# Performance work log

Measured on AMD Instinct MI355X. Metric: run time of the kernel, lower is better.

The kernel has to match this reference:

```python
import jax, jax.numpy as jnp
import numpy as np

B, T, N_EMBD, HEAD = 8, 2048, 1024, 64
NEG_INF = -1e30  # stand-in for float('-inf'), safe under fp16/bf16 after where


def setup_inputs() -> dict:
    key = jax.random.key(0)
    k0, k1, k2, k3 = jax.random.split(key, 4)
    idx = jax.random.normal(k0, (B, T, N_EMBD), dtype=jnp.float32)
    # nn.Linear weights have shape (out_features, in_features)
    Wk = jax.random.normal(k1, (HEAD, N_EMBD), dtype=jnp.float32) * 0.02
    Wq = jax.random.normal(k2, (HEAD, N_EMBD), dtype=jnp.float32) * 0.02
    Wv = jax.random.normal(k3, (HEAD, N_EMBD), dtype=jnp.float32) * 0.02
    return {"idx": idx, "Wk": Wk, "Wq": Wq, "Wv": Wv}


def reference(idx, Wk, Wq, Wv):
    # idx: [B,T,C]; W*: [H,C] (torch Linear layout, y = x @ W.T)
    Tn = idx.shape[1]
    k = jnp.einsum('btc,hc->bth', idx, Wk)
    q = jnp.einsum('btc,hc->bth', idx, Wq)
    v = jnp.einsum('btc,hc->bth', idx, Wv)
    # NOTE: original has NO 1/sqrt(head_size) scaling
    wei = jnp.einsum('bth,bsh->bts', q, k)  # [B,T,T]
    causal = jnp.tril(jnp.ones((Tn, Tn), dtype=bool))  # keep where tril != 0
    wei = jnp.where(causal[None, :, :], wei, NEG_INF)
    # NOTE: original softmaxes over dim=1 (query axis), not the last axis
    wei = jax.nn.softmax(wei, axis=1)
    out = jnp.einsum('bts,bsh->bth', wei, v)  # [B,T,H]
    return out
```

## Files before the change

### kernel.cpp

```cpp
#include <hip/hip_runtime.h>


typedef __attribute__((ext_vector_type(8))) short bf16x8;
typedef __attribute__((ext_vector_type(4))) float f32x4;
typedef unsigned short u16;

#define MFMA(a, b, c) __builtin_amdgcn_mfma_f32_16x16x32_bf16((a), (b), (c), 0, 0, 0)

__device__ __forceinline__ u16 f2bf(float x) {
    unsigned u = __float_as_uint(x);
    u += 0x7fff + ((u >> 16) & 1);
    return (u16)(u >> 16);
}
__device__ __forceinline__ float bf2f(u16 h) {
    return __uint_as_float(((unsigned)h) << 16);
}

#define WH_OFF  0u
#define WL_OFF  (WH_OFF + 192u*1024u*2u)
#define FQH_OFF (WL_OFF + 192u*1024u*2u)
#define FQL_OFF (FQH_OFF + 2u*1024u*1024u)
#define FKH_OFF (FQL_OFF + 2u*1024u*1024u)
#define FKL_OFF (FKH_OFF + 2u*1024u*1024u)
#define VF_OFF  (FKL_OFF + 2u*1024u*1024u)
#define DD_OFF  (VF_OFF + 2u*1024u*1024u)
#define PF_OFF  (DD_OFF + 8u*2048u*4u)

__global__ __launch_bounds__(128) void wsplit_kernel(
    const float* __restrict__ Wk, const float* __restrict__ Wq,
    const float* __restrict__ Wv, u16* __restrict__ FWH, u16* __restrict__ FWL)
{
    const int n = blockIdx.x;
    const int nblk = n >> 4, lr = n & 15;
    const float* src = (n < 64) ? (Wq + (long)n * 1024)
                     : (n < 128) ? (Wk + (long)(n - 64) * 1024)
                                 : (Wv + (long)(n - 128) * 1024);
    const int f = threadIdx.x;
    const int kc = f >> 2, q = f & 3;
    const float4 f0 = *(const float4*)&src[kc * 32 + q * 8];
    const float4 f1 = *(const float4*)&src[kc * 32 + q * 8 + 4];
    const float vs[8] = {f0.x, f0.y, f0.z, f0.w, f1.x, f1.y, f1.z, f1.w};
    bf16x8 hv, lv;
    #pragma unroll
    for (int j = 0; j < 8; ++j) {
        const u16 h = f2bf(vs[j]);
        hv[j] = (short)h;
        lv[j] = (short)f2bf(vs[j] - bf2f(h));
    }
    const long o = ((long)(nblk * 32 + kc) * 64 + q * 16 + lr) * 8;
    *(bf16x8*)&FWH[o] = hv;
    *(bf16x8*)&FWL[o] = lv;
}

__global__ __launch_bounds__(512, 2) void qkv_kernel(
    const float* __restrict__ idx, const u16* __restrict__ FWH, const u16* __restrict__ FWL,
    u16* __restrict__ FQH, u16* __restrict__ FQL,
    u16* __restrict__ FKH, u16* __restrict__ FKL, u16* __restrict__ VF)
{
    __shared__ u16 a_l[2][64 * 136];
    const int tid = threadIdx.x;
    const int w = tid >> 6, lr = tid & 15, quad = (tid >> 4) & 3;
    const int lane = tid & 63;
    const int r0 = blockIdx.x * 64;
    const int b = r0 >> 11, t0 = r0 & 2047;
    const int m0 = (w & 1) * 32;
    const int nbb = (w >> 1) * 3;
    const int sr = tid >> 3, sc = (tid & 7) * 8;
    const float* arow = &idx[(long)(r0 + sr) * 1024 + sc];

    const u16* __restrict__ fwh = &FWH[(long)nbb * 16384 + lane * 8];
    const u16* __restrict__ fwl = &FWL[(long)nbb * 16384 + lane * 8];

    f32x4 acc[2][3] = {};
    float4 pf0, pf1;

    bf16x8 FH0[3][2], FL0[3][2], FH1[3][2], FL1[3][2];
    #pragma unroll
    for (int nf = 0; nf < 3; ++nf) {
        const long nb = (long)nf * 16384;
        FH0[nf][0] = *(const bf16x8*)&fwh[nb];
        FH0[nf][1] = *(const bf16x8*)&fwh[nb + 512];
        FL0[nf][0] = *(const bf16x8*)&fwl[nb];
        FL0[nf][1] = *(const bf16x8*)&fwl[nb + 512];
    }

    pf0 = *(const float4*)(arow);
    pf1 = *(const float4*)(arow + 4);
    {
        const float vs[8] = {pf0.x, pf0.y, pf0.z, pf0.w, pf1.x, pf1.y, pf1.z, pf1.w};
        bf16x8 hv, lv;
        #pragma unroll
        for (int j = 0; j < 8; ++j) {
            const u16 h = f2bf(vs[j]);
            hv[j] = (short)h;
            lv[j] = (short)f2bf(vs[j] - bf2f(h));
        }
        *(bf16x8*)&a_l[0][sr * 136 + sc]      = hv;
        *(bf16x8*)&a_l[0][sr * 136 + 64 + sc] = lv;
    }
    __syncthreads();

    int p = 0;

#define QKV_ITER(IT, FHc, FLc, FHn, FLn)                                      \
    {                                                                         \
        const int it_ = (IT);                                                 \
        if (it_ < 15) {                                                       \
               \
            pf0 = *(const float4*)(arow + it_ * 64 + 64);                     \
            pf1 = *(const float4*)(arow + it_ * 64 + 68);                     \
                                        \
            _Pragma("unroll")                                                 \
            for (int nf = 0; nf < 3; ++nf) {                                  \
                const long nb = (long)nf * 16384 + (long)(it_ + 1) * 1024;    \
                FHn[nf][0] = *(const bf16x8*)&fwh[nb];                        \
                FHn[nf][1] = *(const bf16x8*)&fwh[nb + 512];                  \
                FLn[nf][0] = *(const bf16x8*)&fwl[nb];                        \
                FLn[nf][1] = *(const bf16x8*)&fwl[nb + 512];                  \
            }                                                                 \
        }                                                                     \
        bf16x8 AH[2][2], AL[2][2];                                            \
        _Pragma("unroll")                                                     \
        for (int mi = 0; mi < 2; ++mi) {                                      \
            const int ar = (m0 + mi * 16 + lr) * 136 + quad * 8;              \
            AH[mi][0] = *(const bf16x8*)&a_l[p][ar];                          \
            AH[mi][1] = *(const bf16x8*)&a_l[p][ar + 32];                     \
            AL[mi][0] = *(const bf16x8*)&a_l[p][ar + 64];                     \
            AL[mi][1] = *(const bf16x8*)&a_l[p][ar + 96];                     \
        }                                                                     \
        _Pragma("unroll")                                                     \
        for (int nf = 0; nf < 3; ++nf) {                                      \
            _Pragma("unroll")                                                 \
            for (int mi = 0; mi < 2; ++mi) {                                  \
                f32x4 c = acc[mi][nf];                                        \
                c = MFMA(AH[mi][0], FHc[nf][0], c);                           \
                c = MFMA(AL[mi][0], FHc[nf][0], c);                           \
                c = MFMA(AH[mi][0], FLc[nf][0], c);                           \
                c = MFMA(AH[mi][1], FHc[nf][1], c);                           \
                c = MFMA(AL[mi][1], FHc[nf][1], c);                           \
                c = MFMA(AH[mi][1], FLc[nf][1], c);                           \
                acc[mi][nf] = c;                                              \
            }                                                                 \
        }                                                                     \
        if (it_ < 15) {                                                       \
            const float vs[8] = {pf0.x, pf0.y, pf0.z, pf0.w,                  \
                                 pf1.x, pf1.y, pf1.z, pf1.w};                 \
            bf16x8 hv, lv;                                                    \
            _Pragma("unroll")                                                 \
            for (int j = 0; j < 8; ++j) {                                     \
                const u16 h = f2bf(vs[j]);                                    \
                hv[j] = (short)h;                                             \
                lv[j] = (short)f2bf(vs[j] - bf2f(h));                         \
            }                                                                 \
            *(bf16x8*)&a_l[p ^ 1][sr * 136 + sc]      = hv;                   \
            *(bf16x8*)&a_l[p ^ 1][sr * 136 + 64 + sc] = lv;                   \
            __syncthreads();                                                  \
            p ^= 1;                                                           \
        }                                                                     \
    }

    for (int it2 = 0; it2 < 8; ++it2) {
        QKV_ITER(2 * it2,     FH0, FL0, FH1, FL1);
        QKV_ITER(2 * it2 + 1, FH1, FL1, FH0, FL0);
    }
#undef QKV_ITER

    #pragma unroll
    for (int mi = 0; mi < 2; ++mi) {
        const int tb = t0 + m0 + mi * 16 + quad * 4;
        const int tblk = (t0 + m0 + mi * 16) >> 4;
        #pragma unroll
        for (int nf = 0; nf < 3; ++nf) {
            const int n = (nbb + nf) * 16 + lr;
            const f32x4 a = acc[mi][nf];
            if (n < 128) {
                u16* Hd = (n < 64) ? FQH : FKH;
                u16* Ld = (n < 64) ? FQL : FKL;
                const int h = n & 63;
                const int kc = h >> 5;
                const int lsub = 16 * ((h & 31) >> 3);
                const long base = ((long)(b * 128 + tblk) * 2 + kc) * 512 + (h & 7);
                #pragma unroll
                for (int r = 0; r < 4; ++r) {
                    const float v = a[r];
                    const u16 hi = f2bf(v);
                    const u16 lo = f2bf(v - bf2f(hi));
                    const long o = base + (long)(quad * 4 + r + lsub) * 8;
                    Hd[o] = hi; Ld[o] = lo;
                }
            } else {
                const int h = n - 128;
                const int hblk = h >> 4;
                #pragma unroll
                for (int r = 0; r < 4; ++r) {
                    const int t = tb + r;
                    const long o = ((long)(b * 4 + hblk) * 64 + (t >> 5)) * 512
                                 + (long)(16 * ((t & 31) >> 3) + (h & 15)) * 8 + (t & 7);
                    VF[o] = f2bf(a[r]);
                }
            }
        }
    }
}

__global__ __launch_bounds__(256, 4) void stats_kernel(
    const u16* __restrict__ FQH, const u16* __restrict__ FQL,
    const u16* __restrict__ FKH, const u16* __restrict__ FKL,
    u16* __restrict__ PF, float* __restrict__ D)
{
    __shared__ float red[4][64];
    const int tid = threadIdx.x;
    const int w = tid >> 6, lr = tid & 15, quad = (tid >> 4) & 3;
    const int lane = tid & 63;
    const int b = blockIdx.y;
    int x = blockIdx.x, i = 0;
    for (;;) { const int nc = (35 - i) >> 2; if (x < nc) break; x -= nc; ++i; }
    const int s0 = i * 64;
    const int jt0 = i + 4 * x, jt1 = min(jt0 + 4, 32);

    bf16x8 BH[4][2], BL[4][2];
    #pragma unroll
    for (int nf = 0; nf < 4; ++nf) {
        const long kb = ((long)(b * 128 + i * 4 + nf) * 2) * 512 + lane * 8;
        BH[nf][0] = *(const bf16x8*)&FKH[kb];
        BH[nf][1] = *(const bf16x8*)&FKH[kb + 512];
        BL[nf][0] = *(const bf16x8*)&FKL[kb];
        BL[nf][1] = *(const bf16x8*)&FKL[kb + 512];
    }

    float dsum[4] = {0.f, 0.f, 0.f, 0.f};
    for (int jt = jt0; jt < jt1; ++jt) {
        const long qb = ((long)(b * 128 + jt * 4 + w) * 2) * 512 + lane * 8;
        const bf16x8 ah0 = *(const bf16x8*)&FQH[qb];
        const bf16x8 ah1 = *(const bf16x8*)&FQH[qb + 512];
        const bf16x8 al0 = *(const bf16x8*)&FQL[qb];
        const bf16x8 al1 = *(const bf16x8*)&FQL[qb + 512];
        const bool diag = (jt == i);
        #pragma unroll
        for (int nf = 0; nf < 4; ++nf) {
            f32x4 cc = {};
            cc = MFMA(ah0, BH[nf][0], cc);
            cc = MFMA(al0, BH[nf][0], cc);
            cc = MFMA(ah0, BL[nf][0], cc);
            cc = MFMA(ah1, BH[nf][1], cc);
            cc = MFMA(al1, BH[nf][1], cc);
            cc = MFMA(ah1, BL[nf][1], cc);

            const long pbase = ((long)(b * 128 + jt * 4 + w) * 64 + i * 2 + (nf >> 1)) * 512
                             + (long)(((nf & 1) * 2 + (lr >> 3)) * 16) * 8 + (lr & 7);
            const int sl = nf * 16 + lr;
            #pragma unroll
            for (int r = 0; r < 4; ++r) {
                float ev = __expf(cc[r]);
                if (diag && (w * 16 + quad * 4 + r < sl)) ev = 0.f;
                dsum[nf] += ev;
                PF[pbase + (long)(quad * 4 + r) * 8] = f2bf(ev);
            }
        }
    }

    #pragma unroll
    for (int nf = 0; nf < 4; ++nf) {
        dsum[nf] += __shfl_xor(dsum[nf], 16);
        dsum[nf] += __shfl_xor(dsum[nf], 32);
    }
    if (quad == 0) {
        #pragma unroll
        for (int nf = 0; nf < 4; ++nf) red[w][nf * 16 + lr] = dsum[nf];
    }
    __syncthreads();
    if (tid < 64)
        atomicAdd(&D[b * 2048 + s0 + tid],
                  red[0][tid] + red[1][tid] + red[2][tid] + red[3][tid]);
}

__global__ __launch_bounds__(256) void vscale_kernel(
    u16* __restrict__ VF, const float* __restrict__ D)
{
    const int g = blockIdx.x * 256 + threadIdx.x;
    const long e = (long)g * 8;
    const int lane = (int)((e >> 3) & 63);
    const int kc   = (int)((e >> 9) & 63);
    const int b    = (int)(e >> 17);
    const int s = kc * 32 + (lane >> 4) * 8;
    const float4 d0 = *(const float4*)&D[b * 2048 + s];
    const float4 d1 = *(const float4*)&D[b * 2048 + s + 4];
    const float dv[8] = {d0.x, d0.y, d0.z, d0.w, d1.x, d1.y, d1.z, d1.w};
    bf16x8 vv = *(bf16x8*)&VF[e];
    bf16x8 ov;
    #pragma unroll
    for (int j = 0; j < 8; ++j)
        ov[j] = (short)f2bf(bf2f((u16)vv[j]) / dv[j]);
    *(bf16x8*)&VF[e] = ov;
}

__global__ __launch_bounds__(256, 4) void out_kernel(
    const u16* __restrict__ PF, const u16* __restrict__ VF,
    float* __restrict__ out)
{
    const int tid = threadIdx.x;
    const int w = tid >> 6, lr = tid & 15, quad = (tid >> 4) & 3;
    const int lane = tid & 63;
    const int b = blockIdx.y;
    int x = blockIdx.x, i = 0;
    for (;;) { const int nc = (i + 8) >> 3; if (x < nc) break; x -= nc; ++i; }
    const int t0 = i * 64;
    const int js0 = 8 * x, js1 = min(8 * x + 8, i + 1);
    const int tblk = i * 4 + w;

    f32x4 oacc[4] = {};
    for (int js = js0; js < js1; ++js) {
        const long pb = ((long)(b * 128 + tblk) * 64 + 2 * js) * 512 + lane * 8;
        const bf16x8 a0 = *(const bf16x8*)&PF[pb];
        const bf16x8 a1 = *(const bf16x8*)&PF[pb + 512];
        #pragma unroll
        for (int nf = 0; nf < 4; ++nf) {
            const long vb = ((long)(b * 4 + nf) * 64 + 2 * js) * 512 + lane * 8;
            const bf16x8 v0 = *(const bf16x8*)&VF[vb];
            const bf16x8 v1 = *(const bf16x8*)&VF[vb + 512];
            oacc[nf] = MFMA(a0, v0, oacc[nf]);
            oacc[nf] = MFMA(a1, v1, oacc[nf]);
        }
    }

    const bool single = (i < 8);
    #pragma unroll
    for (int nf = 0; nf < 4; ++nf) {
        const int h = nf * 16 + lr;
        #pragma unroll
        for (int r = 0; r < 4; ++r) {
            const int t = t0 + w * 16 + quad * 4 + r;
            const long o = (long)(b * 2048 + t) * 64 + h;
            if (single) out[o] = oacc[nf][r];
            else        atomicAdd(&out[o], oacc[nf][r]);
        }
    }
}

extern "C" void kernel_launch(void* const* d_in, const int* in_sizes, int n_in,
                              void* d_out, int out_size, void* d_ws, size_t ws_size,
                              hipStream_t stream)
{
    const float* idx = (const float*)d_in[0];
    const float* Wk  = (const float*)d_in[1];
    const float* Wq  = (const float*)d_in[2];
    const float* Wv  = (const float*)d_in[3];
    char* ws = (char*)d_ws;
    float* out = (float*)d_out;

    u16* FWH = (u16*)(ws + WH_OFF);  u16* FWL = (u16*)(ws + WL_OFF);
    u16* FQH = (u16*)(ws + FQH_OFF); u16* FQL = (u16*)(ws + FQL_OFF);
    u16* FKH = (u16*)(ws + FKH_OFF); u16* FKL = (u16*)(ws + FKL_OFF);
    u16* VF  = (u16*)(ws + VF_OFF);
    float* Dp = (float*)(ws + DD_OFF);
    u16* PF  = (u16*)(ws + PF_OFF);

    hipMemsetAsync(out, 0, (size_t)8 * 2048 * 64 * sizeof(float), stream);
    hipMemsetAsync(Dp, 0, (size_t)8 * 2048 * sizeof(float), stream);

    wsplit_kernel<<<192, 128, 0, stream>>>(Wk, Wq, Wv, FWH, FWL);
    qkv_kernel<<<256, 512, 0, stream>>>(idx, FWH, FWL, FQH, FQL, FKH, FKL, VF);
    stats_kernel<<<dim3(144, 8), 256, 0, stream>>>(FQH, FQL, FKH, FKL, PF, Dp);
    vscale_kernel<<<512, 256, 0, stream>>>(VF, Dp);
    out_kernel<<<dim3(80, 8), 256, 0, stream>>>(PF, VF, out);
}
```

Measured before the change: 166.8 us.

## Stage fp32 activations into LDS via direct global-to-LDS loads in QKV projection

The QKV projection now copies raw fp32 idx tiles straight into LDS with global_load_lds, using an XOR-swizzled layout, double-buffered over 128-column K chunks. The bf16 hi/lo split moves to the consumer side, reading from LDS and using a truncating perm-based split instead of round-to-nearest. Weight fragments are loaded per k-block from global memory instead of being prefetched into registers. The goal is to drop the register staging and per-thread conversion on the producer path and to halve the number of barriers. The cost is doubled LDS use (64 KB), conversion work repeated by each wave that reads a tile, and weight loads that are less well hidden.

```diff
diff --git a/kernel.cpp b/kernel.cpp
--- a/kernel.cpp
+++ b/kernel.cpp
@@ -15,6 +15,28 @@
 __device__ __forceinline__ float bf2f(u16 h) {
     return __uint_as_float(((unsigned)h) << 16);
 }
+
+__device__ __forceinline__ void split8(const f32x4 x0, const f32x4 x1,
+                                       bf16x8* hv, bf16x8* lv)
+{
+    const float f[8] = {x0[0], x0[1], x0[2], x0[3], x1[0], x1[1], x1[2], x1[3]};
+    union { unsigned u[4]; bf16x8 v; } H, L;
+    #pragma unroll
+    for (int j = 0; j < 4; ++j) {
+        const unsigned u0 = __float_as_uint(f[2 * j]);
+        const unsigned u1 = __float_as_uint(f[2 * j + 1]);
+        H.u[j] = __builtin_amdgcn_perm(u1, u0, 0x07060302);
+        const float l0 = f[2 * j]     - __uint_as_float(u0 & 0xffff0000u);
+        const float l1 = f[2 * j + 1] - __uint_as_float(u1 & 0xffff0000u);
+        L.u[j] = __builtin_amdgcn_perm(__float_as_uint(l1), __float_as_uint(l0),
+                                       0x07060302);
+    }
+    *hv = H.v;
+    *lv = L.v;
+}
+
+typedef const __attribute__((address_space(1))) void* gas_p;
+typedef __attribute__((address_space(3))) void* las_p;
 
 #define WH_OFF  0u
 #define WL_OFF  (WH_OFF + 192u*1024u*2u)
@@ -57,7 +79,8 @@
     u16* __restrict__ FQH, u16* __restrict__ FQL,
     u16* __restrict__ FKH, u16* __restrict__ FKL, u16* __restrict__ VF)
 {
-    __shared__ u16 a_l[2][64 * 136];
+    __shared__ float a_f0[64 * 128];
+    __shared__ float a_f1[64 * 128];
     const int tid = threadIdx.x;
     const int w = tid >> 6, lr = tid & 15, quad = (tid >> 4) & 3;
     const int lane = tid & 63;
@@ -65,105 +88,74 @@
     const int b = r0 >> 11, t0 = r0 & 2047;
     const int m0 = (w & 1) * 32;
     const int nbb = (w >> 1) * 3;
-    const int sr = tid >> 3, sc = (tid & 7) * 8;
-    const float* arow = &idx[(long)(r0 + sr) * 1024 + sc];
-
-    const u16* __restrict__ fwh = &FWH[(long)nbb * 16384 + lane * 8];
-    const u16* __restrict__ fwl = &FWL[(long)nbb * 16384 + lane * 8];
+
+    const float* gsrc[4];
+    int lseg[4];
+    #pragma unroll
+    for (int g = 0; g < 4; ++g) {
+        const int s = g * 8 + w;
+        const int row = s * 2 + (lane >> 5);
+        const int lc = (lane & 31) ^ (row & 7);
+        gsrc[g] = idx + (long)(r0 + row) * 1024 + lc * 4;
+        lseg[g] = s * 256;
+    }
+
+#define STAGE(BUF, IT)                                                        \
+    {                                                                         \
+        _Pragma("unroll")                                                     \
+        for (int g = 0; g < 4; ++g) {                                         \
+            __builtin_amdgcn_global_load_lds(                                 \
+                (gas_p)(gsrc[g] + (IT) * 128),                                \
+                (las_p)(BUF + lseg[g]), 16, 0, 0);                            \
+        }                                                                     \
+    }
 
     f32x4 acc[2][3] = {};
-    float4 pf0, pf1;
-
-    bf16x8 FH0[3][2], FL0[3][2], FH1[3][2], FL1[3][2];
-    #pragma unroll
-    for (int nf = 0; nf < 3; ++nf) {
-        const long nb = (long)nf * 16384;
-        FH0[nf][0] = *(const bf16x8*)&fwh[nb];
-        FH0[nf][1] = *(const bf16x8*)&fwh[nb + 512];
-        FL0[nf][0] = *(const bf16x8*)&fwl[nb];
-        FL0[nf][1] = *(const bf16x8*)&fwl[nb + 512];
-    }
-
-    pf0 = *(const float4*)(arow);
-    pf1 = *(const float4*)(arow + 4);
-    {
-        const float vs[8] = {pf0.x, pf0.y, pf0.z, pf0.w, pf1.x, pf1.y, pf1.z, pf1.w};
-        bf16x8 hv, lv;
-        #pragma unroll
-        for (int j = 0; j < 8; ++j) {
-            const u16 h = f2bf(vs[j]);
-            hv[j] = (short)h;
-            lv[j] = (short)f2bf(vs[j] - bf2f(h));
-        }
-        *(bf16x8*)&a_l[0][sr * 136 + sc]      = hv;
-        *(bf16x8*)&a_l[0][sr * 136 + 64 + sc] = lv;
-    }
+
+    STAGE(a_f0, 0);
     __syncthreads();
 
-    int p = 0;
-
-#define QKV_ITER(IT, FHc, FLc, FHn, FLn)                                      \
+#define QKV_ITER(IT, BUF, NXT)                                                \
     {                                                                         \
         const int it_ = (IT);                                                 \
-        if (it_ < 15) {                                                       \
-               \
-            pf0 = *(const float4*)(arow + it_ * 64 + 64);                     \
-            pf1 = *(const float4*)(arow + it_ * 64 + 68);                     \
-                                        \
+        if (it_ < 7) STAGE(NXT, it_ + 1);                                     \
+        _Pragma("unroll")                                                     \
+        for (int kblk = 0; kblk < 4; ++kblk) {                                \
+            const int kc = it_ * 4 + kblk;                                    \
+            bf16x8 AH[2], AL[2];                                              \
+            _Pragma("unroll")                                                 \
+            for (int mi = 0; mi < 2; ++mi) {                                  \
+                const int row = m0 + mi * 16 + lr;                            \
+                const int pc0 = (kblk * 8 + quad * 2) ^ (lr & 7);             \
+                const f32x4 x0 = *(const f32x4*)&BUF[row * 128 + pc0 * 4];    \
+                const f32x4 x1 = *(const f32x4*)&BUF[row * 128 + (pc0 ^ 1) * 4]; \
+                split8(x0, x1, &AH[mi], &AL[mi]);                             \
+            }                                                                 \
             _Pragma("unroll")                                                 \
             for (int nf = 0; nf < 3; ++nf) {                                  \
-                const long nb = (long)nf * 16384 + (long)(it_ + 1) * 1024;    \
-                FHn[nf][0] = *(const bf16x8*)&fwh[nb];                        \
-                FHn[nf][1] = *(const bf16x8*)&fwh[nb + 512];                  \
-                FLn[nf][0] = *(const bf16x8*)&fwl[nb];                        \
-                FLn[nf][1] = *(const bf16x8*)&fwl[nb + 512];                  \
+                const long fb = (long)(nbb + nf) * 16384 + (long)kc * 512     \
+                              + lane * 8;                                     \
+                const bf16x8 bh = *(const bf16x8*)&FWH[fb];                   \
+                const bf16x8 bl = *(const bf16x8*)&FWL[fb];                   \
+                _Pragma("unroll")                                             \
+                for (int mi = 0; mi < 2; ++mi) {                              \
+                    f32x4 c = acc[mi][nf];                                    \
+                    c = MFMA(AH[mi], bh, c);                                  \
+                    c = MFMA(AL[mi], bh, c);                                  \
+                    c = MFMA(AH[mi], bl, c);                                  \
+                    acc[mi][nf] = c;                                          \
+                }                                                             \
             }                                                                 \
         }                                                                     \
-        bf16x8 AH[2][2], AL[2][2];                                            \
-        _Pragma("unroll")                                                     \
-        for (int mi = 0; mi < 2; ++mi) {                                      \
-            const int ar = (m0 + mi * 16 + lr) * 136 + quad * 8;              \
-            AH[mi][0] = *(const bf16x8*)&a_l[p][ar];                          \
-            AH[mi][1] = *(const bf16x8*)&a_l[p][ar + 32];                     \
-            AL[mi][0] = *(const bf16x8*)&a_l[p][ar + 64];                     \
-            AL[mi][1] = *(const bf16x8*)&a_l[p][ar + 96];                     \
-        }                                                                     \
-        _Pragma("unroll")                                                     \
-        for (int nf = 0; nf < 3; ++nf) {                                      \
-            _Pragma("unroll")                                                 \
-            for (int mi = 0; mi < 2; ++mi) {                                  \
-                f32x4 c = acc[mi][nf];                                        \
-                c = MFMA(AH[mi][0], FHc[nf][0], c);                           \
-                c = MFMA(AL[mi][0], FHc[nf][0], c);                           \
-                c = MFMA(AH[mi][0], FLc[nf][0], c);                           \
-                c = MFMA(AH[mi][1], FHc[nf][1], c);                           \
-                c = MFMA(AL[mi][1], FHc[nf][1], c);                           \
-                c = MFMA(AH[mi][1], FLc[nf][1], c);                           \
-                acc[mi][nf] = c;                                              \
-            }                                                                 \
-        }                                                                     \
-        if (it_ < 15) {                                                       \
-            const float vs[8] = {pf0.x, pf0.y, pf0.z, pf0.w,                  \
-                                 pf1.x, pf1.y, pf1.z, pf1.w};                 \
-            bf16x8 hv, lv;                                                    \
-            _Pragma("unroll")                                                 \
-            for (int j = 0; j < 8; ++j) {                                     \
-                const u16 h = f2bf(vs[j]);                                    \
-                hv[j] = (short)h;                                             \
-                lv[j] = (short)f2bf(vs[j] - bf2f(h));                         \
-            }                                                                 \
-            *(bf16x8*)&a_l[p ^ 1][sr * 136 + sc]      = hv;                   \
-            *(bf16x8*)&a_l[p ^ 1][sr * 136 + 64 + sc] = lv;                   \
-            __syncthreads();                                                  \
-            p ^= 1;                                                           \
-        }                                                                     \
-    }
-
-    for (int it2 = 0; it2 < 8; ++it2) {
-        QKV_ITER(2 * it2,     FH0, FL0, FH1, FL1);
-        QKV_ITER(2 * it2 + 1, FH1, FL1, FH0, FL0);
+        if (it_ < 7) __syncthreads();                                         \
+    }
+
+    for (int it2 = 0; it2 < 4; ++it2) {
+        QKV_ITER(2 * it2,     a_f0, a_f1);
+        QKV_ITER(2 * it2 + 1, a_f1, a_f0);
     }
 #undef QKV_ITER
+#undef STAGE
 
     #pragma unroll
     for (int mi = 0; mi < 2; ++mi) {
```

Measured after the change: 171.6 us. 1.03x slower.
